# Kernel optimization log

Hardware: AMD Instinct MI355X
Metric: run time of the kernel (lower is better)

## Reference

```python
import jax, jax.numpy as jnp
import numpy as np
import math

D_MODEL, N_HEADS, BATCH, SEQ = 1024, 16, 2, 2048
D_HEAD = D_MODEL // N_HEADS


def setup_inputs() -> dict:
    key = jax.random.key(0)
    ks = jax.random.split(key, 5)
    w = lambda k: jax.random.normal(k, (D_MODEL, D_MODEL), jnp.float32) * 0.02
    return {
        "X": jax.random.normal(ks[0], (BATCH, SEQ, D_MODEL), jnp.float32),
        "W_q": w(ks[1]),
        "W_k": w(ks[2]),
        "W_v": w(ks[3]),
        "W_o": w(ks[4]),
        "g_q": jnp.ones((D_MODEL,), jnp.float32),
        "b_q": jnp.zeros((D_MODEL,), jnp.float32),
        "g_k": jnp.ones((D_MODEL,), jnp.float32),
        "b_k": jnp.zeros((D_MODEL,), jnp.float32),
        "cache_k": jnp.zeros((BATCH, N_HEADS, SEQ, D_HEAD), jnp.float32),
        "cache_v": jnp.zeros((BATCH, N_HEADS, SEQ, D_HEAD), jnp.float32),
        "start_pos": 0,
    }


def _layernorm(x, g, b, eps=1e-5):
    mu = jnp.mean(x, axis=-1, keepdims=True)
    xc = x - mu
    var = jnp.mean(xc * xc, axis=-1, keepdims=True)
    return xc * jax.lax.rsqrt(var + eps) * g + b


def reference(X, W_q, W_k, W_v, W_o, g_q, b_q, g_k, b_k, cache_k, cache_v, start_pos):
    batch, N, d_model = X.shape
    H = cache_k.shape[1]
    dh = d_model // H

    # QK-normed projections (torch Linear: x @ W^T)
    XQ = _layernorm(X @ W_q.T, g_q, b_q)
    XK = _layernorm(X @ W_k.T, g_k, b_k)
    XV = X @ W_v.T
    split = lambda t: t.reshape(batch, N, H, dh).transpose(0, 2, 1, 3)  # [b,h,n,d]
    XQ, XK, XV = split(XQ), split(XK), split(XV)

    # KV-cache scatter update, then slice to valid prefix (start_pos is static)
    cache_k = jax.lax.dynamic_update_slice(cache_k, XK, (0, 0, start_pos, 0))
    cache_v = jax.lax.dynamic_update_slice(cache_v, XV, (0, 0, start_pos, 0))
    M = start_pos + N
    K = cache_k[:, :, :M]
    V = cache_v[:, :, :M]

    logits = jnp.einsum('bhnd,bhmd->bhnm', XQ, K) / math.sqrt(dh)  # [b,h,N,M]

    # causal mask on the freshly written block [start_pos:M]
    tril = jnp.tril(jnp.ones((N, N), bool))
    full_mask = jnp.concatenate([jnp.ones((N, start_pos), bool), tril], axis=1)  # [N,M]
    logits = jnp.where(full_mask[None, None], logits, -jnp.inf)

    # selective forget-mask bias built from relu'd head-0 logits
    S = jax.nn.relu(logits[:, 0])               # relu(-inf) -> 0, matches torch
    S = S.at[..., 0].set(0.0)                   # zero first column
    S = S * (1.0 - jnp.eye(N, dtype=S.dtype))   # zero diagonal (valid since start_pos==0)
    S = jnp.roll(S, 1, axis=-2)                 # shift rows down by one
    S = S.at[..., 0, :].set(0.0)
    F_mask = jnp.cumsum(S, axis=-2)             # [b,N,M]

    logits = logits - F_mask[:, None]
    attn = jax.nn.softmax(logits, axis=-1)
    O = jnp.einsum('bhnm,bhmd->bhnd', attn, V)
    O = O.transpose(0, 2, 1, 3).reshape(batch, N, d_model)
    return O @ W_o.T
```

## Files before the change

kernel.cpp:

```cpp
#include <hip/hip_runtime.h>
#include <cstdint>
#include <cstddef>


typedef unsigned short u16;
typedef __attribute__((ext_vector_type(8))) __bf16 bf16x8;
typedef __attribute__((ext_vector_type(4))) float f32x4;

#define D_MODEL 1024
#define N_HEADS 16
#define BATCH   2
#define SEQ     2048
#define D_HEAD  64
#define ROWS    (BATCH*SEQ)
#define NSEG    64
#define SEGLEN  32
#define LOG2E   1.44269504f

static __device__ __forceinline__ u16 f2bf(float f){
  union { float f; uint32_t u; } v; v.f = f;
  uint32_t r = v.u + 0x7fffu + ((v.u >> 16) & 1u);
  return (u16)(r >> 16);
}
static __device__ __forceinline__ float bf2f(u16 h){
  union { uint32_t u; float f; } v; v.u = ((uint32_t)h) << 16;
  return v.f;
}
static __device__ __forceinline__ uint32_t pack2(float a, float b){
  uint32_t ua = __float_as_uint(a) + 0x8000u;
  uint32_t ub = __float_as_uint(b) + 0x8000u;
  return (ua >> 16) | (ub & 0xffff0000u);
}

__global__ void k_cast_all(const float* __restrict__ X,
                           u16* __restrict__ Xhi, u16* __restrict__ Xlo,
                           const float* __restrict__ Wq,
                           u16* __restrict__ Wqh, u16* __restrict__ Wql,
                           const float* __restrict__ Wk,
                           u16* __restrict__ Wkh, u16* __restrict__ Wkl,
                           const float* __restrict__ Wv, u16* __restrict__ Wvb,
                           const float* __restrict__ Wo, u16* __restrict__ Wob){
  int i = blockIdx.x*256 + threadIdx.x;
  if (i < 1572864){
    const float* src; u16 *dh, *dl; int base;
    if (i < 1048576){ src = X;  dh = Xhi; dl = Xlo; base = i; }
    else if (i < 1310720){ src = Wq; dh = Wqh; dl = Wql; base = i - 1048576; }
    else { src = Wk; dh = Wkh; dl = Wkl; base = i - 1310720; }
    float4 v = reinterpret_cast<const float4*>(src)[base];
    float vs[4] = {v.x, v.y, v.z, v.w};
    union { u16 s[4]; uint2 u; } uh, ul;
#pragma unroll
    for (int r=0;r<4;++r){
      uh.s[r] = f2bf(vs[r]);
      ul.s[r] = f2bf(vs[r] - bf2f(uh.s[r]));
    }
    reinterpret_cast<uint2*>(dh)[base] = uh.u;
    reinterpret_cast<uint2*>(dl)[base] = ul.u;
  } else {
    const float* src; u16* dst; int base;
    if (i < 1835008){ src = Wv; dst = Wvb; base = i - 1572864; }
    else { src = Wo; dst = Wob; base = i - 1835008; }
    float4 v = reinterpret_cast<const float4*>(src)[base];
    float vs[4] = {v.x, v.y, v.z, v.w};
    union { u16 s[4]; uint2 u; } uh;
#pragma unroll
    for (int r=0;r<4;++r) uh.s[r] = f2bf(vs[r]);
    reinterpret_cast<uint2*>(dst)[base] = uh.u;
  }
}

__global__ __launch_bounds__(256) void k_mega(
    const u16* __restrict__ Xhi, const u16* __restrict__ Xlo,
    const u16* __restrict__ Wh,  const u16* __restrict__ Wl,
    const u16* __restrict__ Wvb,
    float* __restrict__ C, float* __restrict__ Dlt, u16* __restrict__ Vt)
{
  __shared__ __align__(16) u16 smem[64*136];
  const int bid = blockIdx.x;
  const int tid = threadIdx.x, wv = tid>>6, ln = tid&63;
  const int lane15 = ln&15, quad = ln>>4;
  const int wm = wv&1, wn = wv>>1;
  const int sRow = ln>>2, sCol = (ln&3)*8;
  f32x4 z = {0.f,0.f,0.f,0.f};

  if (bid < 512){
    u16* As = smem;
    u16* Bs = smem + 4096;
    const size_t rowBase = (size_t)(bid>>4)*128, colBase = (size_t)(bid&15)*128;
    f32x4 acc[4][4];
#pragma unroll
    for (int i=0;i<4;++i)
#pragma unroll
      for (int j=0;j<4;++j) acc[i][j] = z;
    for (int kt = 0; kt < 32; ++kt) {
      __syncthreads();
#pragma unroll
      for (int c = 0; c < 2; ++c) {
        int chunk = wv*2 + c;
        int r = chunk*16 + sRow;
        const u16* ga = Xhi + (rowBase + r)*1024 + kt*32 + sCol;
        const u16* gb = Wh  + (colBase + r)*1024 + kt*32 + sCol;
        __builtin_amdgcn_global_load_lds(
            (const __attribute__((address_space(1))) void*)ga,
            (__attribute__((address_space(3))) void*)(As + chunk*512), 16, 0, 0);
        __builtin_amdgcn_global_load_lds(
            (const __attribute__((address_space(1))) void*)gb,
            (__attribute__((address_space(3))) void*)(Bs + chunk*512), 16, 0, 0);
      }
      __syncthreads();
      bf16x8 af[4], bfb[4];
#pragma unroll
      for (int t=0;t<4;++t){
        af[t]  = *reinterpret_cast<const bf16x8*>(As + (wm*64 + t*16 + lane15)*32 + quad*8);
        bfb[t] = *reinterpret_cast<const bf16x8*>(Bs + (wn*64 + t*16 + lane15)*32 + quad*8);
      }
#pragma unroll
      for (int i=0;i<4;++i)
#pragma unroll
        for (int j=0;j<4;++j)
          acc[i][j] = __builtin_amdgcn_mfma_f32_16x16x32_bf16(af[i], bfb[j], acc[i][j], 0,0,0);
    }
#pragma unroll
    for (int i=0;i<4;++i){
      size_t row = rowBase + wm*64 + i*16 + quad*4;
#pragma unroll
      for (int j=0;j<4;++j){
        size_t col = colBase + wn*64 + j*16 + lane15;
#pragma unroll
        for (int r=0;r<4;++r)
          C[(row+r)*2048 + col] = acc[i][j][r];
      }
    }
  } else if (bid < 640){
    u16* As = smem;
    u16* Bs = smem + 4096;
    const int idx = bid - 512;
    const int cx = idx & 1;
    const int cy = (idx >> 1) & 31;
    const int cz = idx >> 6;
    const size_t rowBase = (size_t)cy*128;
    const size_t wbase = cx ? (size_t)1024*1024 : 0;
    const u16* Ap = cz ? Xlo : Xhi;
    const u16* Bp = (cz ? Wh : Wl) + wbase;
    f32x4 acc[4][2];
#pragma unroll
    for (int i=0;i<4;++i){ acc[i][0] = z; acc[i][1] = z; }
    for (int kt = 0; kt < 32; ++kt) {
      __syncthreads();
#pragma unroll
      for (int c = 0; c < 2; ++c) {
        int chunk = wv*2 + c;
        int r = chunk*16 + sRow;
        const u16* ga = Ap + (rowBase + r)*1024 + kt*32 + sCol;
        __builtin_amdgcn_global_load_lds(
            (const __attribute__((address_space(1))) void*)ga,
            (__attribute__((address_space(3))) void*)(As + chunk*512), 16, 0, 0);
      }
      {
        int r = wv*16 + sRow;
        const u16* gb = Bp + (size_t)r*1024 + kt*32 + sCol;
        __builtin_amdgcn_global_load_lds(
            (const __attribute__((address_space(1))) void*)gb,
            (__attribute__((address_space(3))) void*)(Bs + wv*512), 16, 0, 0);
      }
      __syncthreads();
      bf16x8 af[4], bfb[2];
#pragma unroll
      for (int t=0;t<4;++t)
        af[t]  = *reinterpret_cast<const bf16x8*>(As + (wm*64 + t*16 + lane15)*32 + quad*8);
#pragma unroll
      for (int t=0;t<2;++t)
        bfb[t] = *reinterpret_cast<const bf16x8*>(Bs + (wn*32 + t*16 + lane15)*32 + quad*8);
#pragma unroll
      for (int i=0;i<4;++i)
#pragma unroll
        for (int j=0;j<2;++j)
          acc[i][j] = __builtin_amdgcn_mfma_f32_16x16x32_bf16(af[i], bfb[j], acc[i][j], 0,0,0);
    }
#pragma unroll
    for (int i=0;i<4;++i){
      size_t row = rowBase + wm*64 + i*16 + quad*4;
#pragma unroll
      for (int j=0;j<2;++j){
        size_t col = (size_t)cx*64 + wn*32 + j*16 + lane15;
#pragma unroll
        for (int r=0;r<4;++r)
          atomicAdd(&Dlt[(row+r)*128 + col], acc[i][j][r]);
      }
    }
  } else {
    u16* As = smem;
    u16* Bs = smem + 4096;
    const int idx = bid - 640;
    const int bx = idx & 15, by = idx >> 4;
    const size_t rowBase = (size_t)by*128, colBase = (size_t)bx*64;
    f32x4 acc[4][2];
#pragma unroll
    for (int i=0;i<4;++i){ acc[i][0] = z; acc[i][1] = z; }
    for (int kt = 0; kt < 32; ++kt) {
      __syncthreads();
#pragma unroll
      for (int c = 0; c < 2; ++c) {
        int chunk = wv*2 + c;
        int r = chunk*16 + sRow;
        const u16* ga = Xhi + (rowBase + r)*1024 + kt*32 + sCol;
        __builtin_amdgcn_global_load_lds(
            (const __attribute__((address_space(1))) void*)ga,
            (__attribute__((address_space(3))) void*)(As + chunk*512), 16, 0, 0);
      }
      {
        int r = wv*16 + sRow;
        const u16* gb = Wvb + (colBase + r)*1024 + kt*32 + sCol;
        __builtin_amdgcn_global_load_lds(
            (const __attribute__((address_space(1))) void*)gb,
            (__attribute__((address_space(3))) void*)(Bs + wv*512), 16, 0, 0);
      }
      __syncthreads();
      bf16x8 af[4], bfb[2];
#pragma unroll
      for (int t=0;t<4;++t)
        af[t]  = *reinterpret_cast<const bf16x8*>(As + (wm*64 + t*16 + lane15)*32 + quad*8);
#pragma unroll
      for (int t=0;t<2;++t)
        bfb[t] = *reinterpret_cast<const bf16x8*>(Bs + (wn*32 + t*16 + lane15)*32 + quad*8);
#pragma unroll
      for (int i=0;i<4;++i)
#pragma unroll
        for (int j=0;j<2;++j)
          acc[i][j] = __builtin_amdgcn_mfma_f32_16x16x32_bf16(af[i], bfb[j], acc[i][j], 0,0,0);
    }
    __syncthreads();
#pragma unroll
    for (int i=0;i<4;++i){
      int nl = wm*64 + i*16 + quad*4;
#pragma unroll
      for (int j=0;j<2;++j){
        int dl = wn*32 + j*16 + lane15;
#pragma unroll
        for (int r=0;r<4;++r)
          smem[dl*136 + nl + r] = f2bf(acc[i][j][r]);
      }
    }
    __syncthreads();
    const int b = by >> 4;
    const int n0 = (by & 15) * 128;
    const int bh = b*N_HEADS + bx;
    const int d = tid >> 2, seg = tid & 3;
    u16* dst = Vt + ((size_t)(bh*64 + d))*SEQ + n0 + seg*32;
    const u16* srcl = smem + d*136 + seg*32;
#pragma unroll
    for (int k=0;k<4;++k)
      *reinterpret_cast<uint4*>(dst + k*8) = *reinterpret_cast<const uint4*>(srcl + k*8);
  }
}

__global__ __launch_bounds__(256) void k_ln_pack2(
    const float* __restrict__ C, const float* __restrict__ Dlt,
    const float* __restrict__ gq, const float* __restrict__ bq,
    const float* __restrict__ gk, const float* __restrict__ bk,
    u16* __restrict__ Qh, u16* __restrict__ Kh,
    u16* __restrict__ Q0l, u16* __restrict__ K0l)
{
  const int row = blockIdx.x;
  const int tid = threadIdx.x;
  const float* cr = C + (size_t)row*2048;
  float4 vq = reinterpret_cast<const float4*>(cr)[tid];
  float4 vk = reinterpret_cast<const float4*>(cr)[256 + tid];
  const int h = tid >> 4;
  if (h == 0){
    float4 dq = reinterpret_cast<const float4*>(Dlt + (size_t)row*128)[tid&15];
    vq.x+=dq.x; vq.y+=dq.y; vq.z+=dq.z; vq.w+=dq.w;
    float4 dk = reinterpret_cast<const float4*>(Dlt + (size_t)row*128 + 64)[tid&15];
    vk.x+=dk.x; vk.y+=dk.y; vk.z+=dk.z; vk.w+=dk.w;
  }
  float sq  = vq.x+vq.y+vq.z+vq.w;
  float s2q = vq.x*vq.x+vq.y*vq.y+vq.z*vq.z+vq.w*vq.w;
  float sk  = vk.x+vk.y+vk.z+vk.w;
  float s2k = vk.x*vk.x+vk.y*vk.y+vk.z*vk.z+vk.w*vk.w;
#pragma unroll
  for (int o=32;o;o>>=1){
    sq += __shfl_xor(sq,o);  s2q += __shfl_xor(s2q,o);
    sk += __shfl_xor(sk,o);  s2k += __shfl_xor(s2k,o);
  }
  __shared__ float red[4][4];
  if ((tid&63)==0){
    red[tid>>6][0]=sq; red[tid>>6][1]=s2q; red[tid>>6][2]=sk; red[tid>>6][3]=s2k;
  }
  __syncthreads();
  sq  = red[0][0]+red[1][0]+red[2][0]+red[3][0];
  s2q = red[0][1]+red[1][1]+red[2][1]+red[3][1];
  sk  = red[0][2]+red[1][2]+red[2][2]+red[3][2];
  s2k = red[0][3]+red[1][3]+red[2][3]+red[3][3];
  const float muq = sq*(1.f/D_MODEL);
  const float rsq = rsqrtf(s2q*(1.f/D_MODEL) - muq*muq + 1e-5f);
  const float muk = sk*(1.f/D_MODEL);
  const float rsk = rsqrtf(s2k*(1.f/D_MODEL) - muk*muk + 1e-5f);
  const int b = row >> 11, n = row & (SEQ-1);
  const int d0 = (tid & 15)*4;
  float4 gqv = reinterpret_cast<const float4*>(gq)[tid];
  float4 bqv = reinterpret_cast<const float4*>(bq)[tid];
  float4 gkv = reinterpret_cast<const float4*>(gk)[tid];
  float4 bkv = reinterpret_cast<const float4*>(bk)[tid];
  float xq[4] = {vq.x,vq.y,vq.z,vq.w}, xk[4] = {vk.x,vk.y,vk.z,vk.w};
  float gQ[4] = {gqv.x,gqv.y,gqv.z,gqv.w}, bQ[4] = {bqv.x,bqv.y,bqv.z,bqv.w};
  float gK[4] = {gkv.x,gkv.y,gkv.z,gkv.w}, bK[4] = {bkv.x,bkv.y,bkv.z,bkv.w};
  union { u16 s[4]; uint2 u; } qh, ql, kh, kl;
#pragma unroll
  for (int r=0;r<4;++r){
    float yq = (xq[r]-muq)*rsq*gQ[r] + bQ[r];
    qh.s[r] = f2bf(yq);
    ql.s[r] = f2bf(yq - bf2f(qh.s[r]));
    float yk = (xk[r]-muk)*rsk*gK[r] + bK[r];
    kh.s[r] = f2bf(yk);
    kl.s[r] = f2bf(yk - bf2f(kh.s[r]));
  }
  size_t dst = (((size_t)(b*N_HEADS + h))*SEQ + n)*D_HEAD + d0;
  *reinterpret_cast<uint2*>(Qh + dst) = qh.u;
  *reinterpret_cast<uint2*>(Kh + dst) = kh.u;
  if (h == 0){
    size_t dl = ((size_t)b*SEQ + n)*D_HEAD + d0;
    *reinterpret_cast<uint2*>(Q0l + dl) = ql.u;
    *reinterpret_cast<uint2*>(K0l + dl) = kl.u;
  }
}

__global__ __launch_bounds__(256) void k_s0(
    const u16* Qh, const u16* Q0l, const u16* Kh, const u16* K0l,
    float* __restrict__ S0, float* __restrict__ seg)
{
  const int b = blockIdx.z;
  const int bm = blockIdx.y;
  const int bn = blockIdx.x;
  const int tid = threadIdx.x;
  if (bn > bm){
    for (int t = tid; t < 512; t += 256)
      seg[((size_t)b*NSEG + bm*4 + (t>>7))*SEQ + bn*128 + (t&127)] = 0.f;
    return;
  }
  float* Sb = S0 + (size_t)b*SEQ*SEQ;
  __shared__ __align__(16) u16 As[128*32];
  __shared__ __align__(16) u16 Bs[128*32];
  __shared__ float cs[4][128];
  const int wv = tid>>6, ln = tid&63;
  const int lane15 = ln&15, quad = ln>>4;
  const int wm = wv&1, wn = wv>>1;
  f32x4 acc[4][4];
  f32x4 z = {0.f,0.f,0.f,0.f};
#pragma unroll
  for (int i=0;i<4;++i)
#pragma unroll
    for (int j=0;j<4;++j) acc[i][j] = z;
  const u16* Qb  = Qh  + (size_t)b*N_HEADS*SEQ*D_HEAD;
  const u16* Kb  = Kh  + (size_t)b*N_HEADS*SEQ*D_HEAD;
  const u16* Qlb = Q0l + (size_t)b*SEQ*D_HEAD;
  const u16* Klb = K0l + (size_t)b*SEQ*D_HEAD;
  const u16* Aps[3] = {Qb, Qb, Qlb};
  const u16* Bps[3] = {Kb, Klb, Kb};
  const int sRow = ln>>2, sCol = (ln&3)*8;
  const size_t rowBase = (size_t)bm*128, colBase = (size_t)bn*128;
  for (int p = 0; p < 3; ++p) {
    const u16* Ap = Aps[p];
    const u16* Bp = Bps[p];
    for (int kt = 0; kt < 2; ++kt) {
      __syncthreads();
#pragma unroll
      for (int c = 0; c < 2; ++c) {
        int chunk = wv*2 + c;
        int r = chunk*16 + sRow;
        const u16* ga = Ap + (rowBase + r)*D_HEAD + kt*32 + sCol;
        const u16* gb = Bp + (colBase + r)*D_HEAD + kt*32 + sCol;
        __builtin_amdgcn_global_load_lds(
            (const __attribute__((address_space(1))) void*)ga,
            (__attribute__((address_space(3))) void*)(As + chunk*512), 16, 0, 0);
        __builtin_amdgcn_global_load_lds(
            (const __attribute__((address_space(1))) void*)gb,
            (__attribute__((address_space(3))) void*)(Bs + chunk*512), 16, 0, 0);
      }
      __syncthreads();
      bf16x8 af[4], bfb[4];
#pragma unroll
      for (int t=0;t<4;++t){
        af[t]  = *reinterpret_cast<const bf16x8*>(As + (wm*64 + t*16 + lane15)*32 + quad*8);
        bfb[t] = *reinterpret_cast<const bf16x8*>(Bs + (wn*64 + t*16 + lane15)*32 + quad*8);
      }
#pragma unroll
      for (int i=0;i<4;++i)
#pragma unroll
        for (int j=0;j<4;++j)
          acc[i][j] = __builtin_amdgcn_mfma_f32_16x16x32_bf16(af[i], bfb[j], acc[i][j], 0,0,0);
    }
  }
  float csum[2][4] = {{0.f,0.f,0.f,0.f},{0.f,0.f,0.f,0.f}};
#pragma unroll
  for (int i=0;i<4;++i){
#pragma unroll
    for (int j=0;j<4;++j){
#pragma unroll
      for (int r=0;r<4;++r){
        int jg = (int)rowBase + wm*64 + i*16 + quad*4 + r;
        int mg = (int)colBase + wn*64 + j*16 + lane15;
        float l = acc[i][j][r]*0.125f;
        float s = (mg >= 1 && mg < jg) ? fmaxf(l, 0.f) : 0.f;
        Sb[(size_t)jg*SEQ + mg] = s;
        csum[i>>1][j] += s;
      }
    }
  }
#pragma unroll
  for (int h2=0;h2<2;++h2){
#pragma unroll
    for (int j=0;j<4;++j){
      float v = csum[h2][j];
      v += __shfl_xor(v, 16);
      v += __shfl_xor(v, 32);
      if (ln < 16) cs[wm*2 + h2][wn*64 + j*16 + ln] = v;
    }
  }
  __syncthreads();
  for (int t = tid; t < 512; t += 256)
    seg[((size_t)b*NSEG + bm*4 + (t>>7))*SEQ + bn*128 + (t&127)] = cs[t>>7][t&127];
}

__global__ void k_seg_apply(float* __restrict__ SF, const float* __restrict__ seg){
  int m = blockIdx.x*256 + threadIdx.x;
  int s = blockIdx.y, b = blockIdx.z;
  const float* sb = seg + (size_t)b*NSEG*SEQ;
  float run = 0.f;
  for (int t=0; t<s; ++t) run += sb[(size_t)t*SEQ + m];
  float* Sb = SF + (size_t)b*SEQ*SEQ;
  const int j0 = s*SEGLEN;
#pragma unroll 8
  for (int i=0;i<SEGLEN;++i){
    size_t idx = (size_t)(j0 + i)*SEQ + m;
    float t = Sb[idx];
    Sb[idx] = -run*LOG2E;
    run += (j0 + i > m) ? t : 0.f;
  }
}

__global__ __launch_bounds__(256, 4) void k_attn(
    const u16* __restrict__ Qh, const u16* __restrict__ Kh,
    const u16* __restrict__ Vt, const float* __restrict__ F,
    u16* __restrict__ Ob)
{
  __shared__ __align__(16) u16 Ks[2][64*64];
  __shared__ __align__(16) u16 Vs[2][64*64];
  const int h = blockIdx.x, b = blockIdx.z;
  const int nt = b ? (int)(gridDim.y - 1 - blockIdx.y) : (int)blockIdx.y;
  const int tid = threadIdx.x, wv = tid>>6, ln = tid&63;
  const int lane15 = ln&15, quad = ln>>4;
  const u16* Qbh = Qh + ((size_t)(b*N_HEADS + h))*SEQ*D_HEAD;
  const u16* Kbh = Kh + ((size_t)(b*N_HEADS + h))*SEQ*D_HEAD;
  const u16* Vbh = Vt + ((size_t)(b*N_HEADS + h))*D_HEAD*SEQ;
  const float* Fb = F + (size_t)b*SEQ*SEQ;
  const int n_loc = wv*16 + lane15;
  const int n_g = nt*64 + n_loc;
  const int swz = (ln&7) ^ ((ln>>3)&7);
  const int fswz = lane15 & 7;
  const int srow = ln>>3;

  bf16x8 qf[2];
#pragma unroll
  for (int kt=0; kt<2; ++kt)
    qf[kt] = *reinterpret_cast<const bf16x8*>(Qbh + (size_t)n_g*D_HEAD + kt*32 + quad*8);

  f32x4 z = {0.f,0.f,0.f,0.f};
  f32x4 psum = z;
  f32x4 acc_o[4];
#pragma unroll
  for (int no=0;no<4;++no) acc_o[no] = z;

  auto stage = [&](int mt, int buf){
#pragma unroll
    for (int c=0;c<2;++c){
      int chunk = wv*2 + c;
      int r = chunk*8 + srow;
      const u16* gk = Kbh + (size_t)(mt*64 + r)*D_HEAD + swz*8;
      const u16* gv = Vbh + (size_t)r*SEQ + mt*64 + swz*8;
      __builtin_amdgcn_global_load_lds(
          (const __attribute__((address_space(1))) void*)gk,
          (__attribute__((address_space(3))) void*)(&Ks[buf][chunk*512]), 16, 0, 0);
      __builtin_amdgcn_global_load_lds(
          (const __attribute__((address_space(1))) void*)gv,
          (__attribute__((address_space(3))) void*)(&Vs[buf][chunk*512]), 16, 0, 0);
    }
  };
  stage(0, 0);
  const float c1 = 0.125f*LOG2E;

  for (int mt = 0; mt <= nt; ++mt) {
    const int cur = mt & 1;
    __syncthreads();
    if (mt < nt) stage(mt+1, 1-cur);
    const float* Fr = Fb + (size_t)n_g*SEQ + mt*64;
    f32x4 fv[4];
#pragma unroll
    for (int ms=0; ms<4; ++ms)
      fv[ms] = *reinterpret_cast<const f32x4*>(Fr + ms*16 + quad*4);
    f32x4 accs[4];
#pragma unroll
    for (int ms=0;ms<4;++ms) accs[ms] = z;
#pragma unroll
    for (int kt=0; kt<2; ++kt){
#pragma unroll
      for (int ms=0; ms<4; ++ms){
        bf16x8 a = *reinterpret_cast<const bf16x8*>(
            &Ks[cur][(ms*16 + lane15)*64 + (((kt*4 + quad) ^ fswz) * 8)]);
        accs[ms] = __builtin_amdgcn_mfma_f32_16x16x32_bf16(a, qf[kt], accs[ms], 0,0,0);
      }
    }
    const bool diag = (mt == nt);
    uint32_t pw[4][2];
#pragma unroll
    for (int ms=0; ms<4; ++ms){
      f32x4 t = accs[ms];
      float p[4];
#pragma unroll
      for (int r=0;r<4;++r){
        float l2 = fmaf(t[r], c1, fv[ms][r]);
        if (diag){
          int ml = ms*16 + quad*4 + r;
          l2 = (ml > n_loc) ? -1e30f : l2;
        }
        p[r] = __builtin_amdgcn_exp2f(l2);
      }
      psum[0]+=p[0]; psum[1]+=p[1]; psum[2]+=p[2]; psum[3]+=p[3];
      pw[ms][0] = pack2(p[0], p[1]);
      pw[ms][1] = pack2(p[2], p[3]);
    }
#pragma unroll
    for (int kt=0; kt<2; ++kt){
      union { uint32_t u[4]; bf16x8 v; } pa;
#pragma unroll
      for (int w=0; w<4; ++w){
        int sl = lane15 + 16*((quad&1)*2 + (w>>1));
        uint32_t t0 = (uint32_t)__shfl((int)pw[2*kt  ][w&1], sl);
        uint32_t t1 = (uint32_t)__shfl((int)pw[2*kt+1][w&1], sl);
        pa.u[w] = (quad < 2) ? t0 : t1;
      }
#pragma unroll
      for (int no=0; no<4; ++no){
        int d = no*16 + lane15;
        bf16x8 vb = *reinterpret_cast<const bf16x8*>(
            &Vs[cur][d*64 + (((kt*4 + quad) ^ (d&7)) * 8)]);
        acc_o[no] = __builtin_amdgcn_mfma_f32_16x16x32_bf16(pa.v, vb, acc_o[no], 0,0,0);
      }
    }
  }
  float s = (psum[0]+psum[1]) + (psum[2]+psum[3]);
  s += __shfl_xor(s, 16);
  s += __shfl_xor(s, 32);
  f32x4 inv;
#pragma unroll
  for (int r=0;r<4;++r)
    inv[r] = __builtin_amdgcn_rcpf(__shfl(s, quad*4 + r));
#pragma unroll
  for (int no=0; no<4; ++no){
#pragma unroll
    for (int r=0;r<4;++r){
      float o = acc_o[no][r] * inv[r];
      int row = nt*64 + wv*16 + quad*4 + r;
      Ob[((size_t)(b*SEQ + row))*D_MODEL + h*64 + no*16 + lane15] = f2bf(o);
    }
  }
}

__global__ __launch_bounds__(256) void k_gemm_nt64(
    const u16* __restrict__ A0, const u16* __restrict__ B0,
    float* __restrict__ C, int N, int K)
{
  __shared__ __align__(16) u16 As[128*32];
  __shared__ __align__(16) u16 Bs[64*32];
  const int tid = threadIdx.x, wv = tid>>6, ln = tid&63;
  const int lane15 = ln&15, quad = ln>>4;
  const int wm = wv&1, wn = wv>>1;
  const size_t rowBase = (size_t)blockIdx.y*128, colBase = (size_t)blockIdx.x*64;
  f32x4 acc[4][2];
  f32x4 z = {0.f,0.f,0.f,0.f};
#pragma unroll
  for (int i=0;i<4;++i){ acc[i][0] = z; acc[i][1] = z; }
  const int ktiles = K >> 5;
  const int sRow = ln>>2, sCol = (ln&3)*8;
  for (int kt = 0; kt < ktiles; ++kt) {
    __syncthreads();
#pragma unroll
    for (int c = 0; c < 2; ++c) {
      int chunk = wv*2 + c;
      int r = chunk*16 + sRow;
      const u16* ga = A0 + (rowBase + r)*K + kt*32 + sCol;
      __builtin_amdgcn_global_load_lds(
          (const __attribute__((address_space(1))) void*)ga,
          (__attribute__((address_space(3))) void*)(As + chunk*512), 16, 0, 0);
    }
    {
      int r = wv*16 + sRow;
      const u16* gb = B0 + (colBase + r)*K + kt*32 + sCol;
      __builtin_amdgcn_global_load_lds(
          (const __attribute__((address_space(1))) void*)gb,
          (__attribute__((address_space(3))) void*)(Bs + wv*512), 16, 0, 0);
    }
    __syncthreads();
    bf16x8 af[4], bfb[2];
#pragma unroll
    for (int t=0;t<4;++t)
      af[t]  = *reinterpret_cast<const bf16x8*>(As + (wm*64 + t*16 + lane15)*32 + quad*8);
#pragma unroll
    for (int t=0;t<2;++t)
      bfb[t] = *reinterpret_cast<const bf16x8*>(Bs + (wn*32 + t*16 + lane15)*32 + quad*8);
#pragma unroll
    for (int i=0;i<4;++i)
#pragma unroll
      for (int j=0;j<2;++j)
        acc[i][j] = __builtin_amdgcn_mfma_f32_16x16x32_bf16(af[i], bfb[j], acc[i][j], 0,0,0);
  }
#pragma unroll
  for (int i=0;i<4;++i){
    size_t row = rowBase + wm*64 + i*16 + quad*4;
#pragma unroll
    for (int j=0;j<2;++j){
      size_t col = colBase + wn*32 + j*16 + lane15;
#pragma unroll
      for (int r=0;r<4;++r)
        C[(row+r)*N + col] = acc[i][j][r];
    }
  }
}

extern "C" void kernel_launch(void* const* d_in, const int* in_sizes, int n_in,
                              void* d_out, int out_size, void* d_ws, size_t ws_size,
                              hipStream_t stream)
{
  (void)in_sizes; (void)n_in; (void)out_size; (void)ws_size;
  const float* X  = (const float*)d_in[0];
  const float* Wq = (const float*)d_in[1];
  const float* Wk = (const float*)d_in[2];
  const float* Wv = (const float*)d_in[3];
  const float* Wo = (const float*)d_in[4];
  const float* gq = (const float*)d_in[5];
  const float* bq = (const float*)d_in[6];
  const float* gk = (const float*)d_in[7];
  const float* bk = (const float*)d_in[8];
  float* out = (float*)d_out;

  char* ws = (char*)d_ws;
  size_t off = 0;
  auto alloc = [&](size_t bytes)->char*{
    char* p = ws + off; off += (bytes + 255) & ~(size_t)255; return p;
  };
  u16* Xhi  = (u16*)alloc((size_t)ROWS*D_MODEL*2);
  u16* Xlo  = (u16*)alloc((size_t)ROWS*D_MODEL*2);
  u16* Wqkh = (u16*)alloc((size_t)2*D_MODEL*D_MODEL*2);
  u16* Wqkl = (u16*)alloc((size_t)2*D_MODEL*D_MODEL*2);
  u16* Wvb  = (u16*)alloc((size_t)D_MODEL*D_MODEL*2);
  u16* Wob  = (u16*)alloc((size_t)D_MODEL*D_MODEL*2);
  u16* Qhp  = (u16*)alloc((size_t)BATCH*N_HEADS*SEQ*D_HEAD*2);
  u16* Khp  = (u16*)alloc((size_t)BATCH*N_HEADS*SEQ*D_HEAD*2);
  u16* Q0l  = (u16*)alloc((size_t)BATCH*SEQ*D_HEAD*2);
  u16* K0l  = (u16*)alloc((size_t)BATCH*SEQ*D_HEAD*2);
  u16* Vtp  = (u16*)alloc((size_t)BATCH*N_HEADS*D_HEAD*SEQ*2);
  u16* Obf  = (u16*)alloc((size_t)ROWS*D_MODEL*2);
  float* Dlt = (float*)alloc((size_t)ROWS*128*4);
  float* Seg = (float*)alloc((size_t)BATCH*NSEG*SEQ*4);
  float* SF  = (float*)alloc((size_t)BATCH*SEQ*SEQ*4);
  float* C32 = SF;

  hipMemsetAsync(Dlt, 0, (size_t)ROWS*128*4, stream);

  k_cast_all<<<8192, 256, 0, stream>>>(
      X, Xhi, Xlo,
      Wq, Wqkh, Wqkl,
      Wk, Wqkh + (size_t)D_MODEL*D_MODEL, Wqkl + (size_t)D_MODEL*D_MODEL,
      Wv, Wvb, Wo, Wob);

  k_mega<<<1152, 256, 0, stream>>>(Xhi, Xlo, Wqkh, Wqkl, Wvb, C32, Dlt, Vtp);

  k_ln_pack2<<<ROWS, 256, 0, stream>>>(C32, Dlt, gq, bq, gk, bk, Qhp, Khp, Q0l, K0l);
  k_s0<<<dim3(16, 16, BATCH), 256, 0, stream>>>(Qhp, Q0l, Khp, K0l, SF, Seg);
  k_seg_apply<<<dim3(8, NSEG, BATCH), 256, 0, stream>>>(SF, Seg);
  k_attn<<<dim3(N_HEADS, SEQ/64, BATCH), 256, 0, stream>>>(Qhp, Khp, Vtp, SF, Obf);
  k_gemm_nt64<<<dim3(16, 32), 256, 0, stream>>>(Obf, Wob, out, D_MODEL, D_MODEL);
}
```

Baseline: 311.9 us.

## Use K=64 XOR-swizzled LDS tiles, reorder mega blocks, prefetch F rows

```diff
diff --git a/kernel.cpp b/kernel.cpp
--- a/kernel.cpp
+++ b/kernel.cpp
@@ -31,6 +31,9 @@
   uint32_t ub = __float_as_uint(b) + 0x8000u;
   return (ua >> 16) | (ub & 0xffff0000u);
 }
+#define GLDS(gp, lp) __builtin_amdgcn_global_load_lds( \
+    (const __attribute__((address_space(1))) void*)(gp), \
+    (__attribute__((address_space(3))) void*)(lp), 16, 0, 0)
 
 __global__ void k_cast_all(const float* __restrict__ X,
                            u16* __restrict__ Xhi, u16* __restrict__ Xlo,
@@ -75,69 +78,21 @@
     const u16* __restrict__ Wvb,
     float* __restrict__ C, float* __restrict__ Dlt, u16* __restrict__ Vt)
 {
-  __shared__ __align__(16) u16 smem[64*136];
+  __shared__ __align__(16) u16 smem[16384];
   const int bid = blockIdx.x;
   const int tid = threadIdx.x, wv = tid>>6, ln = tid&63;
   const int lane15 = ln&15, quad = ln>>4;
   const int wm = wv&1, wn = wv>>1;
-  const int sRow = ln>>2, sCol = (ln&3)*8;
+  const int g = ln&7, sr = ln>>3;
+  const int fs = lane15 & 7;
   f32x4 z = {0.f,0.f,0.f,0.f};
-
-  if (bid < 512){
-    u16* As = smem;
-    u16* Bs = smem + 4096;
-    const size_t rowBase = (size_t)(bid>>4)*128, colBase = (size_t)(bid&15)*128;
-    f32x4 acc[4][4];
-#pragma unroll
-    for (int i=0;i<4;++i)
-#pragma unroll
-      for (int j=0;j<4;++j) acc[i][j] = z;
-    for (int kt = 0; kt < 32; ++kt) {
-      __syncthreads();
-#pragma unroll
-      for (int c = 0; c < 2; ++c) {
-        int chunk = wv*2 + c;
-        int r = chunk*16 + sRow;
-        const u16* ga = Xhi + (rowBase + r)*1024 + kt*32 + sCol;
-        const u16* gb = Wh  + (colBase + r)*1024 + kt*32 + sCol;
-        __builtin_amdgcn_global_load_lds(
-            (const __attribute__((address_space(1))) void*)ga,
-            (__attribute__((address_space(3))) void*)(As + chunk*512), 16, 0, 0);
-        __builtin_amdgcn_global_load_lds(
-            (const __attribute__((address_space(1))) void*)gb,
-            (__attribute__((address_space(3))) void*)(Bs + chunk*512), 16, 0, 0);
-      }
-      __syncthreads();
-      bf16x8 af[4], bfb[4];
-#pragma unroll
-      for (int t=0;t<4;++t){
-        af[t]  = *reinterpret_cast<const bf16x8*>(As + (wm*64 + t*16 + lane15)*32 + quad*8);
-        bfb[t] = *reinterpret_cast<const bf16x8*>(Bs + (wn*64 + t*16 + lane15)*32 + quad*8);
-      }
-#pragma unroll
-      for (int i=0;i<4;++i)
-#pragma unroll
-        for (int j=0;j<4;++j)
-          acc[i][j] = __builtin_amdgcn_mfma_f32_16x16x32_bf16(af[i], bfb[j], acc[i][j], 0,0,0);
-    }
-#pragma unroll
-    for (int i=0;i<4;++i){
-      size_t row = rowBase + wm*64 + i*16 + quad*4;
-#pragma unroll
-      for (int j=0;j<4;++j){
-        size_t col = colBase + wn*64 + j*16 + lane15;
-#pragma unroll
-        for (int r=0;r<4;++r)
-          C[(row+r)*2048 + col] = acc[i][j][r];
-      }
-    }
-  } else if (bid < 640){
-    u16* As = smem;
-    u16* Bs = smem + 4096;
-    const int idx = bid - 512;
-    const int cx = idx & 1;
-    const int cy = (idx >> 1) & 31;
-    const int cz = idx >> 6;
+  u16* As = smem;
+  u16* Bs = smem + 8192;
+
+  if (bid < 128){
+    const int cx = bid & 1;
+    const int cy = (bid >> 1) & 31;
+    const int cz = bid >> 6;
     const size_t rowBase = (size_t)cy*128;
     const size_t wbase = cx ? (size_t)1024*1024 : 0;
     const u16* Ap = cz ? Xlo : Xhi;
@@ -145,37 +100,34 @@
     f32x4 acc[4][2];
 #pragma unroll
     for (int i=0;i<4;++i){ acc[i][0] = z; acc[i][1] = z; }
-    for (int kt = 0; kt < 32; ++kt) {
+    for (int kt = 0; kt < 16; ++kt) {
       __syncthreads();
 #pragma unroll
+      for (int c = 0; c < 4; ++c) {
+        int chunk = wv*4 + c, r = chunk*8 + sr;
+        GLDS(Ap + (rowBase + r)*1024 + kt*64 + (g^sr)*8, As + chunk*512);
+      }
+#pragma unroll
       for (int c = 0; c < 2; ++c) {
-        int chunk = wv*2 + c;
-        int r = chunk*16 + sRow;
-        const u16* ga = Ap + (rowBase + r)*1024 + kt*32 + sCol;
-        __builtin_amdgcn_global_load_lds(
-            (const __attribute__((address_space(1))) void*)ga,
-            (__attribute__((address_space(3))) void*)(As + chunk*512), 16, 0, 0);
-      }
-      {
-        int r = wv*16 + sRow;
-        const u16* gb = Bp + (size_t)r*1024 + kt*32 + sCol;
-        __builtin_amdgcn_global_load_lds(
-            (const __attribute__((address_space(1))) void*)gb,
-            (__attribute__((address_space(3))) void*)(Bs + wv*512), 16, 0, 0);
+        int chunk = wv*2 + c, r = chunk*8 + sr;
+        GLDS(Bp + (size_t)r*1024 + kt*64 + (g^sr)*8, Bs + chunk*512);
       }
       __syncthreads();
-      bf16x8 af[4], bfb[2];
-#pragma unroll
-      for (int t=0;t<4;++t)
-        af[t]  = *reinterpret_cast<const bf16x8*>(As + (wm*64 + t*16 + lane15)*32 + quad*8);
-#pragma unroll
-      for (int t=0;t<2;++t)
-        bfb[t] = *reinterpret_cast<const bf16x8*>(Bs + (wn*32 + t*16 + lane15)*32 + quad*8);
-#pragma unroll
-      for (int i=0;i<4;++i)
-#pragma unroll
-        for (int j=0;j<2;++j)
-          acc[i][j] = __builtin_amdgcn_mfma_f32_16x16x32_bf16(af[i], bfb[j], acc[i][j], 0,0,0);
+#pragma unroll
+      for (int k2=0;k2<2;++k2){
+        bf16x8 af[4], bfb[2];
+#pragma unroll
+        for (int t=0;t<4;++t)
+          af[t]  = *reinterpret_cast<const bf16x8*>(As + (wm*64 + t*16 + lane15)*64 + (((k2*4+quad)^fs)*8));
+#pragma unroll
+        for (int t=0;t<2;++t)
+          bfb[t] = *reinterpret_cast<const bf16x8*>(Bs + (wn*32 + t*16 + lane15)*64 + (((k2*4+quad)^fs)*8));
+#pragma unroll
+        for (int i=0;i<4;++i)
+#pragma unroll
+          for (int j=0;j<2;++j)
+            acc[i][j] = __builtin_amdgcn_mfma_f32_16x16x32_bf16(af[i], bfb[j], acc[i][j], 0,0,0);
+      }
     }
 #pragma unroll
     for (int i=0;i<4;++i){
@@ -188,46 +140,84 @@
           atomicAdd(&Dlt[(row+r)*128 + col], acc[i][j][r]);
       }
     }
+  } else if (bid < 640){
+    const int idx = bid - 128;
+    const size_t rowBase = (size_t)(idx>>4)*128, colBase = (size_t)(idx&15)*128;
+    f32x4 acc[4][4];
+#pragma unroll
+    for (int i=0;i<4;++i)
+#pragma unroll
+      for (int j=0;j<4;++j) acc[i][j] = z;
+    for (int kt = 0; kt < 16; ++kt) {
+      __syncthreads();
+#pragma unroll
+      for (int c = 0; c < 4; ++c) {
+        int chunk = wv*4 + c, r = chunk*8 + sr;
+        GLDS(Xhi + (rowBase + r)*1024 + kt*64 + (g^sr)*8, As + chunk*512);
+        GLDS(Wh  + (colBase + r)*1024 + kt*64 + (g^sr)*8, Bs + chunk*512);
+      }
+      __syncthreads();
+#pragma unroll
+      for (int k2=0;k2<2;++k2){
+        bf16x8 af[4], bfb[4];
+#pragma unroll
+        for (int t=0;t<4;++t){
+          af[t]  = *reinterpret_cast<const bf16x8*>(As + (wm*64 + t*16 + lane15)*64 + (((k2*4+quad)^fs)*8));
+          bfb[t] = *reinterpret_cast<const bf16x8*>(Bs + (wn*64 + t*16 + lane15)*64 + (((k2*4+quad)^fs)*8));
+        }
+#pragma unroll
+        for (int i=0;i<4;++i)
+#pragma unroll
+          for (int j=0;j<4;++j)
+            acc[i][j] = __builtin_amdgcn_mfma_f32_16x16x32_bf16(af[i], bfb[j], acc[i][j], 0,0,0);
+      }
+    }
+#pragma unroll
+    for (int i=0;i<4;++i){
+      size_t row = rowBase + wm*64 + i*16 + quad*4;
+#pragma unroll
+      for (int j=0;j<4;++j){
+        size_t col = colBase + wn*64 + j*16 + lane15;
+#pragma unroll
+        for (int r=0;r<4;++r)
+          C[(row+r)*2048 + col] = acc[i][j][r];
+      }
+    }
   } else {
-    u16* As = smem;
-    u16* Bs = smem + 4096;
     const int idx = bid - 640;
     const int bx = idx & 15, by = idx >> 4;
     const size_t rowBase = (size_t)by*128, colBase = (size_t)bx*64;
     f32x4 acc[4][2];
 #pragma unroll
     for (int i=0;i<4;++i){ acc[i][0] = z; acc[i][1] = z; }
-    for (int kt = 0; kt < 32; ++kt) {
+    for (int kt = 0; kt < 16; ++kt) {
       __syncthreads();
 #pragma unroll
+      for (int c = 0; c < 4; ++c) {
+        int chunk = wv*4 + c, r = chunk*8 + sr;
+        GLDS(Xhi + (rowBase + r)*1024 + kt*64 + (g^sr)*8, As + chunk*512);
+      }
+#pragma unroll
       for (int c = 0; c < 2; ++c) {
-        int chunk = wv*2 + c;
-        int r = chunk*16 + sRow;
-        const u16* ga = Xhi + (rowBase + r)*1024 + kt*32 + sCol;
-        __builtin_amdgcn_global_load_lds(
-            (const __attribute__((address_space(1))) void*)ga,
-            (__attribute__((address_space(3))) void*)(As + chunk*512), 16, 0, 0);
-      }
-      {
-        int r = wv*16 + sRow;
-        const u16* gb = Wvb + (colBase + r)*1024 + kt*32 + sCol;
-        __builtin_amdgcn_global_load_lds(
-            (const __attribute__((address_space(1))) void*)gb,
-            (__attribute__((address_space(3))) void*)(Bs + wv*512), 16, 0, 0);
+        int chunk = wv*2 + c, r = chunk*8 + sr;
+        GLDS(Wvb + (colBase + r)*1024 + kt*64 + (g^sr)*8, Bs + chunk*512);
       }
       __syncthreads();
-      bf16x8 af[4], bfb[2];
-#pragma unroll
-      for (int t=0;t<4;++t)
-        af[t]  = *reinterpret_cast<const bf16x8*>(As + (wm*64 + t*16 + lane15)*32 + quad*8);
-#pragma unroll
-      for (int t=0;t<2;++t)
-        bfb[t] = *reinterpret_cast<const bf16x8*>(Bs + (wn*32 + t*16 + lane15)*32 + quad*8);
-#pragma unroll
-      for (int i=0;i<4;++i)
-#pragma unroll
-        for (int j=0;j<2;++j)
-          acc[i][j] = __builtin_amdgcn_mfma_f32_16x16x32_bf16(af[i], bfb[j], acc[i][j], 0,0,0);
+#pragma unroll
+      for (int k2=0;k2<2;++k2){
+        bf16x8 af[4], bfb[2];
+#pragma unroll
+        for (int t=0;t<4;++t)
+          af[t]  = *reinterpret_cast<const bf16x8*>(As + (wm*64 + t*16 + lane15)*64 + (((k2*4+quad)^fs)*8));
+#pragma unroll
+        for (int t=0;t<2;++t)
+          bfb[t] = *reinterpret_cast<const bf16x8*>(Bs + (wn*32 + t*16 + lane15)*64 + (((k2*4+quad)^fs)*8));
+#pragma unroll
+        for (int i=0;i<4;++i)
+#pragma unroll
+          for (int j=0;j<2;++j)
+            acc[i][j] = __builtin_amdgcn_mfma_f32_16x16x32_bf16(af[i], bfb[j], acc[i][j], 0,0,0);
+      }
     }
     __syncthreads();
 #pragma unroll
@@ -338,50 +328,46 @@
     return;
   }
   float* Sb = S0 + (size_t)b*SEQ*SEQ;
-  __shared__ __align__(16) u16 As[128*32];
-  __shared__ __align__(16) u16 Bs[128*32];
-  __shared__ float cs[4][128];
+  __shared__ __align__(16) u16 smem[4*8192];
   const int wv = tid>>6, ln = tid&63;
   const int lane15 = ln&15, quad = ln>>4;
   const int wm = wv&1, wn = wv>>1;
+  const int g = ln&7, sr = ln>>3;
+  const int fs = lane15 & 7;
+  const size_t rowBase = (size_t)bm*128, colBase = (size_t)bn*128;
+  const u16* srcs[4] = {
+    Qh  + ((size_t)b*N_HEADS*SEQ + rowBase)*D_HEAD,
+    Q0l + ((size_t)b*SEQ + rowBase)*D_HEAD,
+    Kh  + ((size_t)b*N_HEADS*SEQ + colBase)*D_HEAD,
+    K0l + ((size_t)b*SEQ + colBase)*D_HEAD };
+#pragma unroll
+  for (int t=0;t<4;++t){
+#pragma unroll
+    for (int c=0;c<4;++c){
+      int chunk = wv*4 + c, r = chunk*8 + sr;
+      GLDS(srcs[t] + (size_t)r*64 + (g^sr)*8, smem + t*8192 + chunk*512);
+    }
+  }
+  __syncthreads();
   f32x4 acc[4][4];
   f32x4 z = {0.f,0.f,0.f,0.f};
 #pragma unroll
   for (int i=0;i<4;++i)
 #pragma unroll
     for (int j=0;j<4;++j) acc[i][j] = z;
-  const u16* Qb  = Qh  + (size_t)b*N_HEADS*SEQ*D_HEAD;
-  const u16* Kb  = Kh  + (size_t)b*N_HEADS*SEQ*D_HEAD;
-  const u16* Qlb = Q0l + (size_t)b*SEQ*D_HEAD;
-  const u16* Klb = K0l + (size_t)b*SEQ*D_HEAD;
-  const u16* Aps[3] = {Qb, Qb, Qlb};
-  const u16* Bps[3] = {Kb, Klb, Kb};
-  const int sRow = ln>>2, sCol = (ln&3)*8;
-  const size_t rowBase = (size_t)bm*128, colBase = (size_t)bn*128;
-  for (int p = 0; p < 3; ++p) {
-    const u16* Ap = Aps[p];
-    const u16* Bp = Bps[p];
-    for (int kt = 0; kt < 2; ++kt) {
-      __syncthreads();
-#pragma unroll
-      for (int c = 0; c < 2; ++c) {
-        int chunk = wv*2 + c;
-        int r = chunk*16 + sRow;
-        const u16* ga = Ap + (rowBase + r)*D_HEAD + kt*32 + sCol;
-        const u16* gb = Bp + (colBase + r)*D_HEAD + kt*32 + sCol;
-        __builtin_amdgcn_global_load_lds(
-            (const __attribute__((address_space(1))) void*)ga,
-            (__attribute__((address_space(3))) void*)(As + chunk*512), 16, 0, 0);
-        __builtin_amdgcn_global_load_lds(
-            (const __attribute__((address_space(1))) void*)gb,
-            (__attribute__((address_space(3))) void*)(Bs + chunk*512), 16, 0, 0);
-      }
-      __syncthreads();
+  const int Aidx[3] = {0, 0, 1};
+  const int Bidx[3] = {2, 3, 2};
+#pragma unroll
+  for (int p = 0; p < 3; ++p){
+    const u16* At = smem + Aidx[p]*8192;
+    const u16* Bt = smem + Bidx[p]*8192;
+#pragma unroll
+    for (int k2=0;k2<2;++k2){
       bf16x8 af[4], bfb[4];
 #pragma unroll
       for (int t=0;t<4;++t){
-        af[t]  = *reinterpret_cast<const bf16x8*>(As + (wm*64 + t*16 + lane15)*32 + quad*8);
-        bfb[t] = *reinterpret_cast<const bf16x8*>(Bs + (wn*64 + t*16 + lane15)*32 + quad*8);
+        af[t]  = *reinterpret_cast<const bf16x8*>(At + (wm*64 + t*16 + lane15)*64 + (((k2*4+quad)^fs)*8));
+        bfb[t] = *reinterpret_cast<const bf16x8*>(Bt + (wn*64 + t*16 + lane15)*64 + (((k2*4+quad)^fs)*8));
       }
 #pragma unroll
       for (int i=0;i<4;++i)
@@ -406,6 +392,8 @@
       }
     }
   }
+  __syncthreads();
+  float* cs = (float*)smem;
 #pragma unroll
   for (int h2=0;h2<2;++h2){
 #pragma unroll
@@ -413,12 +401,12 @@
       float v = csum[h2][j];
       v += __shfl_xor(v, 16);
       v += __shfl_xor(v, 32);
-      if (ln < 16) cs[wm*2 + h2][wn*64 + j*16 + ln] = v;
+      if (ln < 16) cs[(wm*2 + h2)*128 + wn*64 + j*16 + ln] = v;
     }
   }
   __syncthreads();
   for (int t = tid; t < 512; t += 256)
-    seg[((size_t)b*NSEG + bm*4 + (t>>7))*SEQ + bn*128 + (t&127)] = cs[t>>7][t&127];
+    seg[((size_t)b*NSEG + bm*4 + (t>>7))*SEQ + bn*128 + (t&127)] = cs[t];
 }
 
 __global__ void k_seg_apply(float* __restrict__ SF, const float* __restrict__ seg){
@@ -452,9 +440,9 @@
   const u16* Qbh = Qh + ((size_t)(b*N_HEADS + h))*SEQ*D_HEAD;
   const u16* Kbh = Kh + ((size_t)(b*N_HEADS + h))*SEQ*D_HEAD;
   const u16* Vbh = Vt + ((size_t)(b*N_HEADS + h))*D_HEAD*SEQ;
-  const float* Fb = F + (size_t)b*SEQ*SEQ;
   const int n_loc = wv*16 + lane15;
   const int n_g = nt*64 + n_loc;
+  const float* Frow = F + (size_t)b*SEQ*SEQ + (size_t)n_g*SEQ;
   const int swz = (ln&7) ^ ((ln>>3)&7);
   const int fswz = lane15 & 7;
   const int srow = ln>>3;
@@ -475,28 +463,30 @@
     for (int c=0;c<2;++c){
       int chunk = wv*2 + c;
       int r = chunk*8 + srow;
-      const u16* gk = Kbh + (size_t)(mt*64 + r)*D_HEAD + swz*8;
-      const u16* gv = Vbh + (size_t)r*SEQ + mt*64 + swz*8;
-      __builtin_amdgcn_global_load_lds(
-          (const __attribute__((address_space(1))) void*)gk,
-          (__attribute__((address_space(3))) void*)(&Ks[buf][chunk*512]), 16, 0, 0);
-      __builtin_amdgcn_global_load_lds(
-          (const __attribute__((address_space(1))) void*)gv,
-          (__attribute__((address_space(3))) void*)(&Vs[buf][chunk*512]), 16, 0, 0);
+      GLDS(Kbh + (size_t)(mt*64 + r)*D_HEAD + swz*8, &Ks[buf][chunk*512]);
+      GLDS(Vbh + (size_t)r*SEQ + mt*64 + swz*8,      &Vs[buf][chunk*512]);
     }
   };
   stage(0, 0);
+  f32x4 fvn[4];
+#pragma unroll
+  for (int ms=0; ms<4; ++ms)
+    fvn[ms] = *reinterpret_cast<const f32x4*>(Frow + ms*16 + quad*4);
   const float c1 = 0.125f*LOG2E;
 
   for (int mt = 0; mt <= nt; ++mt) {
     const int cur = mt & 1;
     __syncthreads();
     if (mt < nt) stage(mt+1, 1-cur);
-    const float* Fr = Fb + (size_t)n_g*SEQ + mt*64;
     f32x4 fv[4];
 #pragma unroll
-    for (int ms=0; ms<4; ++ms)
-      fv[ms] = *reinterpret_cast<const f32x4*>(Fr + ms*16 + quad*4);
+    for (int ms=0; ms<4; ++ms) fv[ms] = fvn[ms];
+    if (mt < nt){
+      const float* Fr1 = Frow + (mt+1)*64;
+#pragma unroll
+      for (int ms=0; ms<4; ++ms)
+        fvn[ms] = *reinterpret_cast<const f32x4*>(Fr1 + ms*16 + quad*4);
+    }
     f32x4 accs[4];
 #pragma unroll
     for (int ms=0;ms<4;++ms) accs[ms] = z;
@@ -569,49 +559,47 @@
     const u16* __restrict__ A0, const u16* __restrict__ B0,
     float* __restrict__ C, int N, int K)
 {
-  __shared__ __align__(16) u16 As[128*32];
-  __shared__ __align__(16) u16 Bs[64*32];
+  __shared__ __align__(16) u16 As[8192];
+  __shared__ __align__(16) u16 Bs[4096];
   const int tid = threadIdx.x, wv = tid>>6, ln = tid&63;
   const int lane15 = ln&15, quad = ln>>4;
   const int wm = wv&1, wn = wv>>1;
+  const int g = ln&7, sr = ln>>3;
+  const int fs = lane15 & 7;
   const size_t rowBase = (size_t)blockIdx.y*128, colBase = (size_t)blockIdx.x*64;
   f32x4 acc[4][2];
   f32x4 z = {0.f,0.f,0.f,0.f};
 #pragma unroll
   for (int i=0;i<4;++i){ acc[i][0] = z; acc[i][1] = z; }
-  const int ktiles = K >> 5;
-  const int sRow = ln>>2, sCol = (ln&3)*8;
+  const int ktiles = K >> 6;
   for (int kt = 0; kt < ktiles; ++kt) {
     __syncthreads();
 #pragma unroll
+    for (int c = 0; c < 4; ++c) {
+      int chunk = wv*4 + c, r = chunk*8 + sr;
+      GLDS(A0 + (rowBase + r)*K + kt*64 + (g^sr)*8, As + chunk*512);
+    }
+#pragma unroll
     for (int c = 0; c < 2; ++c) {
-      int chunk = wv*2 + c;
-      int r = chunk*16 + sRow;
-      const u16* ga = A0 + (rowBase + r)*K + kt*32 + sCol;
-      __builtin_amdgcn_global_load_lds(
-          (const __attribute__((address_space(1))) void*)ga,
-          (__attribute__((address_space(3))) void*)(As + chunk*512), 16, 0, 0);
-    }
-    {
-      int r = wv*16 + sRow;
-      const u16* gb = B0 + (colBase + r)*K + kt*32 + sCol;
-      __builtin_amdgcn_global_load_lds(
-          (const __attribute__((address_space(1))) void*)gb,
-          (__attribute__((address_space(3))) void*)(Bs + wv*512), 16, 0, 0);
+      int chunk = wv*2 + c, r = chunk*8 + sr;
+      GLDS(B0 + (colBase + r)*K + kt*64 + (g^sr)*8, Bs + chunk*512);
     }
     __syncthreads();
-    bf16x8 af[4], bfb[2];
-#pragma unroll
-    for (int t=0;t<4;++t)
-      af[t]  = *reinterpret_cast<const bf16x8*>(As + (wm*64 + t*16 + lane15)*32 + quad*8);
-#pragma unroll
-    for (int t=0;t<2;++t)
-      bfb[t] = *reinterpret_cast<const bf16x8*>(Bs + (wn*32 + t*16 + lane15)*32 + quad*8);
-#pragma unroll
-    for (int i=0;i<4;++i)
-#pragma unroll
-      for (int j=0;j<2;++j)
-        acc[i][j] = __builtin_amdgcn_mfma_f32_16x16x32_bf16(af[i], bfb[j], acc[i][j], 0,0,0);
+#pragma unroll
+    for (int k2=0;k2<2;++k2){
+      bf16x8 af[4], bfb[2];
+#pragma unroll
+      for (int t=0;t<4;++t)
+        af[t]  = *reinterpret_cast<const bf16x8*>(As + (wm*64 + t*16 + lane15)*64 + (((k2*4+quad)^fs)*8));
+#pragma unroll
+      for (int t=0;t<2;++t)
+        bfb[t] = *reinterpret_cast<const bf16x8*>(Bs + (wn*32 + t*16 + lane15)*64 + (((k2*4+quad)^fs)*8));
+#pragma unroll
+      for (int i=0;i<4;++i)
+#pragma unroll
+        for (int j=0;j<2;++j)
+          acc[i][j] = __builtin_amdgcn_mfma_f32_16x16x32_bf16(af[i], bfb[j], acc[i][j], 0,0,0);
+    }
   }
 #pragma unroll
   for (int i=0;i<4;++i){
@@ -671,9 +659,7 @@
       Wq, Wqkh, Wqkl,
       Wk, Wqkh + (size_t)D_MODEL*D_MODEL, Wqkl + (size_t)D_MODEL*D_MODEL,
       Wv, Wvb, Wo, Wob);
-
   k_mega<<<1152, 256, 0, stream>>>(Xhi, Xlo, Wqkh, Wqkl, Wvb, C32, Dlt, Vtp);
-
   k_ln_pack2<<<ROWS, 256, 0, stream>>>(C32, Dlt, gq, bq, gk, bk, Qhp, Khp, Q0l, K0l);
   k_s0<<<dim3(16, 16, BATCH), 256, 0, stream>>>(Qhp, Q0l, Khp, K0l, SF, Seg);
   k_seg_apply<<<dim3(8, NSEG, BATCH), 256, 0, stream>>>(SF, Seg);
```

After: 291.6 us. 6.5% less time.
